# Performance work log

Measured on AMD Instinct MI355X. Metric: run time of the kernel, lower is better.

Reference implementation:

```python
import jax, jax.numpy as jnp
import numpy as np
from jax import lax

VOCAB, EMB, HID = 50257, 256, 256
B, T = 64, 2048

def setup_inputs() -> dict:
    key = jax.random.key(0)
    ks = jax.random.split(key, 6)
    s = 1.0 / np.sqrt(HID)
    return {
        "sequence": jax.random.randint(ks[0], (B, T), 0, VOCAB),
        "embedding": jax.random.normal(ks[1], (VOCAB, EMB), jnp.float32),
        "w_ih": jax.random.uniform(ks[2], (3 * HID, EMB), jnp.float32, -s, s),
        "w_hh": jax.random.uniform(ks[3], (3 * HID, HID), jnp.float32, -s, s),
        "b_ih": jax.random.uniform(ks[4], (3 * HID,), jnp.float32, -s, s),
        "b_hh": jax.random.uniform(ks[5], (3 * HID,), jnp.float32, -s, s),
    }

def reference(sequence, embedding, w_ih, w_hh, b_ih, b_hh):
    # sequence: [B,T] int tokens. Original loops per-timestep; math == one GRU pass.
    H = w_hh.shape[1]
    x = embedding[sequence]                       # [B,T,E]
    x = jnp.transpose(x, (1, 0, 2))               # [T,B,E] (time-major)
    # input-side gate pre-activations for all steps at once: [T,B,3H]
    gi = jnp.einsum('tbe,ge->tbg', x, w_ih) + b_ih

    def step(h, gi_t):
        gh = h @ w_hh.T + b_hh                    # [B,3H]
        i_r, i_z, i_n = jnp.split(gi_t, 3, axis=-1)
        h_r, h_z, h_n = jnp.split(gh, 3, axis=-1)
        r = jax.nn.sigmoid(i_r + h_r)
        z = jax.nn.sigmoid(i_z + h_z)
        n = jnp.tanh(i_n + r * h_n)
        h_new = (1.0 - z) * n + z * h
        return h_new, None

    h0 = jnp.zeros((sequence.shape[0], H), dtype=embedding.dtype)
    hT, _ = lax.scan(step, h0, gi)
    return hT[None]                                # [1,B,H] like torch GRU hidden
```

## Files before the change

### kernel.cpp

```cpp
#include <hip/hip_runtime.h>
#include <hip/hip_fp16.h>

#define TSEQ   2048
#define NB     64
#define NE     256
#define NH     256
#define NG     768
#define TCH    64
#define NCHUNK (TSEQ / TCH)
#define POOL_BYTES 87552

__global__ void prep_whh(const float* __restrict__ whh, unsigned int* __restrict__ w16) {
  int idx = blockIdx.x * 256 + threadIdx.x;
  if (idx >= 98304) return;
  int c  = idx & 3;
  int i  = (idx >> 2) & 15;
  int g  = (idx >> 6) % 3;
  int js = idx / 192;
  int s  = js & 1;
  int j  = js >> 1;
  int k  = s * 128 + i * 8 + 2 * c;
  const float* src = whh + (size_t)(g * 256 + j) * 256 + k;
  union { struct { _Float16 a, b; } h; unsigned int u; } cvt;
  cvt.h.a = (_Float16)src[0];
  cvt.h.b = (_Float16)src[1];
  w16[idx] = cvt.u;
}

#define DOT12(H0,H1,H2,H3,R0,R1,R2,R3,Z0,Z1,Z2,Z3,N0,N1,N2,N3) \
  "v_dot2_f32_f16 v16, v" H0 ", v" R0 ", v16\n\t" \
  "v_dot2_f32_f16 v17, v" H0 ", v" Z0 ", v17\n\t" \
  "v_dot2_f32_f16 v18, v" H0 ", v" N0 ", v18\n\t" \
  "v_dot2_f32_f16 v16, v" H1 ", v" R1 ", v16\n\t" \
  "v_dot2_f32_f16 v17, v" H1 ", v" Z1 ", v17\n\t" \
  "v_dot2_f32_f16 v18, v" H1 ", v" N1 ", v18\n\t" \
  "v_dot2_f32_f16 v16, v" H2 ", v" R2 ", v16\n\t" \
  "v_dot2_f32_f16 v17, v" H2 ", v" Z2 ", v17\n\t" \
  "v_dot2_f32_f16 v18, v" H2 ", v" N2 ", v18\n\t" \
  "v_dot2_f32_f16 v16, v" H3 ", v" R3 ", v16\n\t" \
  "v_dot2_f32_f16 v17, v" H3 ", v" Z3 ", v17\n\t" \
  "v_dot2_f32_f16 v18, v" H3 ", v" N3 ", v18\n\t"

#define TAIL(CA0,CA1,CA2,WOF) \
  "ds_bpermute_b32 v20, v19, v16\n\t" \
  "ds_bpermute_b32 v21, v19, v17\n\t" \
  "ds_bpermute_b32 v22, v19, v18\n\t" \
  "s_waitcnt lgkmcnt(0)\n\t" \
  "v_add_f32 v16, v16, v20\n\t" \
  "v_add_f32 v17, v17, v21\n\t" \
  "v_add_f32 v18, v18, v22\n\t" \
  "s_waitcnt vmcnt(3)\n\t" \
  "v_add_f32 v20, v" CA0 ", v16\n\t" \
  "v_mul_f32 v20, 0xbfb8aa3b, v20\n\t" \
  "v_exp_f32 v20, v20\n\t" \
  "s_nop 0\n\t" \
  "v_add_f32 v20, 1.0, v20\n\t" \
  "v_rcp_f32 v20, v20\n\t" \
  "s_nop 0\n\t" \
  "v_add_f32 v21, v" CA1 ", v17\n\t" \
  "v_mul_f32 v21, 0xbfb8aa3b, v21\n\t" \
  "v_exp_f32 v21, v21\n\t" \
  "s_nop 0\n\t" \
  "v_add_f32 v21, 1.0, v21\n\t" \
  "v_rcp_f32 v21, v21\n\t" \
  "s_nop 0\n\t" \
  "v_add_f32 v22, v18, v28\n\t" \
  "v_fma_f32 v22, v20, v22, v" CA2 "\n\t" \
  "v_min_f32 v22, 0x41700000, v22\n\t" \
  "v_mul_f32 v22, 0x4038aa3b, v22\n\t" \
  "v_exp_f32 v22, v22\n\t" \
  "s_nop 0\n\t" \
  "v_add_f32 v23, -1.0, v22\n\t" \
  "v_add_f32 v22, 1.0, v22\n\t" \
  "v_rcp_f32 v22, v22\n\t" \
  "s_nop 0\n\t" \
  "v_mul_f32 v22, v23, v22\n\t" \
  "v_sub_f32 v23, v24, v22\n\t" \
  "v_fma_f32 v24, v21, v23, v22\n\t" \
  "v_cvt_f16_f32 v25, v24\n\t" \
  "ds_write_b16 v29, v25 offset:" WOF "\n\t" \
  "s_waitcnt lgkmcnt(0)\n\t" \
  "s_barrier\n\t"

#define STEP(O0,O1,O2,O3,O4,O5,O6,O7,O8,O9,O10,O11,O12,O13,O14,O15,CA0,CA1,CA2,PB0,PB1,PB2,WOF) \
  "ds_read_b128 v[32:35], v2 offset:" O0 "\n\t" \
  "ds_read_b128 v[36:39], v2 offset:" O1 "\n\t" \
  "ds_read_b128 v[40:43], v2 offset:" O2 "\n\t" \
  "ds_read_b128 v[44:47], v2 offset:" O3 "\n\t" \
  "ds_read_b128 v[48:51], v2 offset:" O4 "\n\t" \
  "ds_read_b128 v[52:55], v2 offset:" O5 "\n\t" \
  "ds_read_b128 v[56:59], v2 offset:" O6 "\n\t" \
  "ds_read_b128 v[60:63], v2 offset:" O7 "\n\t" \
  "global_load_dword v" PB0 ", v3, %[gip]\n\t" \
  "global_load_dword v" PB1 ", v3, %[gip] offset:1024\n\t" \
  "global_load_dword v" PB2 ", v3, %[gip] offset:2048\n\t" \
  "v_add_u32 v3, 0x30000, v3\n\t" \
  "v_mov_b32 v16, 0\n\t" \
  "v_mov_b32 v17, 0\n\t" \
  "v_mov_b32 v18, 0\n\t" \
  "s_waitcnt lgkmcnt(7)\n\t" \
  DOT12("32","33","34","35","64","65","66","67","128","129","130","131","192","193","194","195") \
  "ds_read_b128 v[32:35], v2 offset:" O8 "\n\t" \
  "s_waitcnt lgkmcnt(7)\n\t" \
  DOT12("36","37","38","39","68","69","70","71","132","133","134","135","196","197","198","199") \
  "ds_read_b128 v[36:39], v2 offset:" O9 "\n\t" \
  "s_waitcnt lgkmcnt(7)\n\t" \
  DOT12("40","41","42","43","72","73","74","75","136","137","138","139","200","201","202","203") \
  "ds_read_b128 v[40:43], v2 offset:" O10 "\n\t" \
  "s_waitcnt lgkmcnt(7)\n\t" \
  DOT12("44","45","46","47","76","77","78","79","140","141","142","143","204","205","206","207") \
  "ds_read_b128 v[44:47], v2 offset:" O11 "\n\t" \
  "s_waitcnt lgkmcnt(7)\n\t" \
  DOT12("48","49","50","51","80","81","82","83","144","145","146","147","208","209","210","211") \
  "ds_read_b128 v[48:51], v2 offset:" O12 "\n\t" \
  "s_waitcnt lgkmcnt(7)\n\t" \
  DOT12("52","53","54","55","84","85","86","87","148","149","150","151","212","213","214","215") \
  "ds_read_b128 v[52:55], v2 offset:" O13 "\n\t" \
  "s_waitcnt lgkmcnt(7)\n\t" \
  DOT12("56","57","58","59","88","89","90","91","152","153","154","155","216","217","218","219") \
  "ds_read_b128 v[56:59], v2 offset:" O14 "\n\t" \
  "s_waitcnt lgkmcnt(7)\n\t" \
  DOT12("60","61","62","63","92","93","94","95","156","157","158","159","220","221","222","223") \
  "ds_read_b128 v[60:63], v2 offset:" O15 "\n\t" \
  "s_waitcnt lgkmcnt(7)\n\t" \
  DOT12("32","33","34","35","96","97","98","99","160","161","162","163","224","225","226","227") \
  "s_waitcnt lgkmcnt(6)\n\t" \
  DOT12("36","37","38","39","100","101","102","103","164","165","166","167","228","229","230","231") \
  "s_waitcnt lgkmcnt(5)\n\t" \
  DOT12("40","41","42","43","104","105","106","107","168","169","170","171","232","233","234","235") \
  "s_waitcnt lgkmcnt(4)\n\t" \
  DOT12("44","45","46","47","108","109","110","111","172","173","174","175","236","237","238","239") \
  "s_waitcnt lgkmcnt(3)\n\t" \
  DOT12("48","49","50","51","112","113","114","115","176","177","178","179","240","241","242","243") \
  "s_waitcnt lgkmcnt(2)\n\t" \
  DOT12("52","53","54","55","116","117","118","119","180","181","182","183","244","245","246","247") \
  "s_waitcnt lgkmcnt(1)\n\t" \
  DOT12("56","57","58","59","120","121","122","123","184","185","186","187","248","249","250","251") \
  "s_waitcnt lgkmcnt(0)\n\t" \
  DOT12("60","61","62","63","124","125","126","127","188","189","190","191","252","253","254","255") \
  TAIL(CA0,CA1,CA2,WOF)

#define WLD(D0,D1,OFF) \
  "global_load_dwordx4 v[" D0 ":" D1 "], %[wof], %[wptr] offset:" OFF "\n\t"

__global__ __launch_bounds__(512)
void fused_kernel(const int* __restrict__ seq, const float* __restrict__ emb,
                  const float* __restrict__ wih, const float* __restrict__ bih,
                  const float* __restrict__ bhh, const unsigned int* __restrict__ w16,
                  const float* __restrict__ rec_gi, float* __restrict__ gi_dst,
                  int gi_t0, float* __restrict__ h_state, float* __restrict__ out,
                  int rec_count, int chunk)
{
  __shared__ __align__(16) char smem[POOL_BYTES];
  const int tid = threadIdx.x;

  if ((int)blockIdx.x < rec_count) {
    const int b = blockIdx.x;
    const unsigned lane = tid & 63;
    const unsigned jj   = (unsigned)(tid >> 6) * 32 + (lane & 31);
    const unsigned sh   = lane >> 5;

    float h0 = 0.f;
    if (chunk != 0) h0 = h_state[b * NH + jj];
    const float bnv = bhh[2 * NH + jj];
    ((_Float16*)smem)[jj] = (_Float16)h0;
    __syncthreads();

    const unsigned pool0 = (unsigned)(uintptr_t)(smem);
    const unsigned hrd = pool0 + sh * 256;
    const unsigned hwa = pool0 + jj * 2;
    const unsigned gio = jj * 4;
    const unsigned bpa = (lane ^ 32u) << 2;
    const unsigned wof = (jj * 2 + sh) * 768;
    const float* gib = rec_gi + (size_t)b * NG;

    float hout;
    asm volatile(
      "v_mov_b32 v2, %[hrd]\n\t"
      "v_mov_b32 v3, %[gio]\n\t"
      "v_mov_b32 v19, %[bpa]\n\t"
      "v_mov_b32 v24, %[h0]\n\t"
      "v_mov_b32 v28, %[bn]\n\t"
      "v_mov_b32 v29, %[hwa]\n\t"
      WLD("64","67","0")    WLD("68","71","16")   WLD("72","75","32")   WLD("76","79","48")
      WLD("80","83","64")   WLD("84","87","80")   WLD("88","91","96")   WLD("92","95","112")
      WLD("96","99","128")  WLD("100","103","144")WLD("104","107","160")WLD("108","111","176")
      WLD("112","115","192")WLD("116","119","208")WLD("120","123","224")WLD("124","127","240")
      WLD("128","131","256")WLD("132","135","272")WLD("136","139","288")WLD("140","143","304")
      WLD("144","147","320")WLD("148","151","336")WLD("152","155","352")WLD("156","159","368")
      WLD("160","163","384")WLD("164","167","400")WLD("168","171","416")WLD("172","175","432")
      WLD("176","179","448")WLD("180","183","464")WLD("184","187","480")WLD("188","191","496")
      WLD("192","195","512")WLD("196","199","528")WLD("200","203","544")WLD("204","207","560")
      WLD("208","211","576")WLD("212","215","592")WLD("216","219","608")WLD("220","223","624")
      WLD("224","227","640")WLD("228","231","656")WLD("232","235","672")WLD("236","239","688")
      WLD("240","243","704")WLD("244","247","720")WLD("248","251","736")WLD("252","255","752")
      "s_waitcnt vmcnt(0)\n\t"
      "global_load_dword v12, v3, %[gip]\n\t"
      "global_load_dword v13, v3, %[gip] offset:1024\n\t"
      "global_load_dword v14, v3, %[gip] offset:2048\n\t"
      "v_add_u32 v3, 0x30000, v3\n\t"
      "s_mov_b32 s20, 32\n\t"
      "1:\n\t"
      STEP("0","16","32","48","64","80","96","112",
           "128","144","160","176","192","208","224","240",
           "12","13","14","26","27","30","512")
      STEP("512","528","544","560","576","592","608","624",
           "640","656","672","688","704","720","736","752",
           "26","27","30","12","13","14","0")
      "s_sub_u32 s20, s20, 1\n\t"
      "s_cmp_lg_u32 s20, 0\n\t"
      "s_cbranch_scc1 1b\n\t"
      "v_mov_b32 %[hout], v24\n\t"
      : [hout] "=v"(hout)
      : [hrd] "v"(hrd), [gio] "v"(gio), [bpa] "v"(bpa), [h0] "v"(h0),
        [bn] "v"(bnv), [hwa] "v"(hwa), [wof] "v"(wof),
        [wptr] "s"(w16), [gip] "s"(gib)
      : "memory","scc","s20",
        "v2","v3","v12","v13","v14","v16","v17","v18","v19","v20","v21","v22",
        "v23","v24","v25","v26","v27","v28","v29","v30",
        "v32","v33","v34","v35","v36","v37","v38","v39","v40","v41","v42","v43",
        "v44","v45","v46","v47","v48","v49","v50","v51","v52","v53","v54","v55",
        "v56","v57","v58","v59","v60","v61","v62","v63",
        "v64","v65","v66","v67","v68","v69","v70","v71","v72","v73","v74","v75",
        "v76","v77","v78","v79","v80","v81","v82","v83","v84","v85","v86","v87",
        "v88","v89","v90","v91","v92","v93","v94","v95","v96","v97","v98","v99",
        "v100","v101","v102","v103","v104","v105","v106","v107","v108","v109",
        "v110","v111","v112","v113","v114","v115","v116","v117","v118","v119",
        "v120","v121","v122","v123","v124","v125","v126","v127","v128","v129",
        "v130","v131","v132","v133","v134","v135","v136","v137","v138","v139",
        "v140","v141","v142","v143","v144","v145","v146","v147","v148","v149",
        "v150","v151","v152","v153","v154","v155","v156","v157","v158","v159",
        "v160","v161","v162","v163","v164","v165","v166","v167","v168","v169",
        "v170","v171","v172","v173","v174","v175","v176","v177","v178","v179",
        "v180","v181","v182","v183","v184","v185","v186","v187","v188","v189",
        "v190","v191","v192","v193","v194","v195","v196","v197","v198","v199",
        "v200","v201","v202","v203","v204","v205","v206","v207","v208","v209",
        "v210","v211","v212","v213","v214","v215","v216","v217","v218","v219",
        "v220","v221","v222","v223","v224","v225","v226","v227","v228","v229",
        "v230","v231","v232","v233","v234","v235","v236","v237","v238","v239",
        "v240","v241","v242","v243","v244","v245","v246","v247","v248","v249",
        "v250","v251","v252","v253","v254","v255");

    h_state[b * NH + jj] = hout;
    if (out) out[b * NH + jj] = hout;
  } else {
    if (gi_dst == nullptr) return;
    float (*xs)[68]  = (float(*)[68])smem;
    float (*wsh)[68] = (float(*)[68])(smem + 17408);
    int*  tok        = (int*)(smem + 17408 + 69632);
    const int gb = blockIdx.x - rec_count;
    const int tl = gb & 63;
    const int g0 = (gb >> 6) * 256;
    const int t  = gi_t0 + tl;
    if (tid < 64) tok[tid] = seq[tid * TSEQ + t];
    const int tx = tid & 31;
    const int ty = tid >> 5;
    float acc[4][8];
#pragma unroll
    for (int i = 0; i < 4; ++i)
#pragma unroll
      for (int c8 = 0; c8 < 8; ++c8) acc[i][c8] = 0.f;

    for (int kb = 0; kb < 4; ++kb) {
      __syncthreads();
#pragma unroll
      for (int it = 0; it < 2; ++it) {
        int i = it * 512 + tid;
        int r = i >> 4, c = i & 15;
        *(float4*)(&xs[r][c * 4]) =
            *(const float4*)(emb + (size_t)tok[r] * NE + kb * 64 + c * 4);
      }
#pragma unroll
      for (int it = 0; it < 8; ++it) {
        int i = it * 512 + tid;
        int r = i >> 4, c = i & 15;
        *(float4*)(&wsh[r][c * 4]) =
            *(const float4*)(wih + (size_t)(g0 + r) * NE + kb * 64 + c * 4);
      }
      __syncthreads();
#pragma unroll 4
      for (int k4 = 0; k4 < 16; ++k4) {
        float4 xf[4], wf[8];
#pragma unroll
        for (int i = 0; i < 4; ++i) xf[i] = *(const float4*)(&xs[ty * 4 + i][k4 * 4]);
#pragma unroll
        for (int c8 = 0; c8 < 8; ++c8) wf[c8] = *(const float4*)(&wsh[tx + 32 * c8][k4 * 4]);
#pragma unroll
        for (int i = 0; i < 4; ++i)
#pragma unroll
          for (int c8 = 0; c8 < 8; ++c8)
            acc[i][c8] += xf[i].x * wf[c8].x + xf[i].y * wf[c8].y +
                          xf[i].z * wf[c8].z + xf[i].w * wf[c8].w;
      }
    }
#pragma unroll
    for (int i = 0; i < 4; ++i) {
      const int brow = ty * 4 + i;
      float* dst = gi_dst + ((size_t)(tl * NB + brow)) * NG + g0;
#pragma unroll
      for (int c8 = 0; c8 < 8; ++c8) {
        const int col = tx + 32 * c8;
        const int g = g0 + col;
        float bias = bih[g] + (g < 2 * NH ? bhh[g] : 0.f);
        dst[col] = acc[i][c8] + bias;
      }
    }
  }
}

extern "C" void kernel_launch(void* const* d_in, const int* in_sizes, int n_in,
                              void* d_out, int out_size, void* d_ws, size_t ws_size,
                              hipStream_t stream) {
  (void)in_sizes; (void)n_in; (void)out_size; (void)ws_size;
  const int*   seq = (const int*)d_in[0];
  const float* emb = (const float*)d_in[1];
  const float* wih = (const float*)d_in[2];
  const float* whh = (const float*)d_in[3];
  const float* bih = (const float*)d_in[4];
  const float* bhh = (const float*)d_in[5];
  float* out = (float*)d_out;
  char*  ws  = (char*)d_ws;

  unsigned int* w16     = (unsigned int*)(ws);
  float*        h_state = (float*)(ws + 393216);
  float*        gi0     = (float*)(ws + 458752);
  float*        gi1     = (float*)(ws + 458752 + 12582912);

  prep_whh<<<dim3(384), dim3(256), 0, stream>>>(whh, w16);

  fused_kernel<<<dim3(192), dim3(512), 0, stream>>>(
      seq, emb, wih, bih, bhh, w16,
      nullptr, gi0, 0, h_state, nullptr, 0, 0);

  for (int c = 0; c < NCHUNK; ++c) {
    float* rd  = (c & 1) ? gi1 : gi0;
    float* wr_ = (c & 1) ? gi0 : gi1;
    const bool last = (c == NCHUNK - 1);
    const int grid  = last ? NB : NB + 192;
    fused_kernel<<<dim3(grid), dim3(512), 0, stream>>>(
        seq, emb, wih, bih, bhh, w16,
        rd, last ? nullptr : wr_, (c + 1) * TCH, h_state,
        last ? out : nullptr, NB, c);
  }
}
```

Baseline: 2.631 ms.

## Split fused recurrence/projection kernel into separate rec and gi kernels

Replaces the single fused kernel, which ran recurrence blocks and next-chunk input-projection blocks in one grid, with two kernels launched back to back per chunk. The recurrence kernel now needs only 2 KB of shared memory instead of the large shared pool. The aim is to stop the projection blocks from contending with the latency-bound recurrence blocks. The cost is that the projection work is no longer overlapped with the recurrence, and the launch count per chunk doubles.

```diff
diff --git a/kernel.cpp b/kernel.cpp
--- a/kernel.cpp
+++ b/kernel.cpp
@@ -8,7 +8,6 @@
 #define NG     768
 #define TCH    64
 #define NCHUNK (TSEQ / TCH)
-#define POOL_BYTES 87552
 
 __global__ void prep_whh(const float* __restrict__ whh, unsigned int* __restrict__ w16) {
   int idx = blockIdx.x * 256 + threadIdx.x;
@@ -144,166 +143,169 @@
   "global_load_dwordx4 v[" D0 ":" D1 "], %[wof], %[wptr] offset:" OFF "\n\t"
 
 __global__ __launch_bounds__(512)
-void fused_kernel(const int* __restrict__ seq, const float* __restrict__ emb,
-                  const float* __restrict__ wih, const float* __restrict__ bih,
-                  const float* __restrict__ bhh, const unsigned int* __restrict__ w16,
-                  const float* __restrict__ rec_gi, float* __restrict__ gi_dst,
-                  int gi_t0, float* __restrict__ h_state, float* __restrict__ out,
-                  int rec_count, int chunk)
+void rec_kernel(const unsigned int* __restrict__ w16,
+                const float* __restrict__ rec_gi,
+                const float* __restrict__ bhh,
+                float* __restrict__ h_state, float* __restrict__ out,
+                int chunk)
 {
-  __shared__ __align__(16) char smem[POOL_BYTES];
+  __shared__ __align__(16) char smem[2048];
   const int tid = threadIdx.x;
-
-  if ((int)blockIdx.x < rec_count) {
-    const int b = blockIdx.x;
-    const unsigned lane = tid & 63;
-    const unsigned jj   = (unsigned)(tid >> 6) * 32 + (lane & 31);
-    const unsigned sh   = lane >> 5;
-
-    float h0 = 0.f;
-    if (chunk != 0) h0 = h_state[b * NH + jj];
-    const float bnv = bhh[2 * NH + jj];
-    ((_Float16*)smem)[jj] = (_Float16)h0;
+  const int b = blockIdx.x;
+  const unsigned lane = tid & 63;
+  const unsigned jj   = (unsigned)(tid >> 6) * 32 + (lane & 31);
+  const unsigned sh   = lane >> 5;
+
+  float h0 = 0.f;
+  if (chunk != 0) h0 = h_state[b * NH + jj];
+  const float bnv = bhh[2 * NH + jj];
+  ((_Float16*)smem)[jj] = (_Float16)h0;
+  __syncthreads();
+
+  const unsigned pool0 = (unsigned)(uintptr_t)(smem);
+  const unsigned hrd = pool0 + sh * 256;
+  const unsigned hwa = pool0 + jj * 2;
+  const unsigned gio = jj * 4;
+  const unsigned bpa = (lane ^ 32u) << 2;
+  const unsigned wof = (jj * 2 + sh) * 768;
+  const float* gib = rec_gi + (size_t)b * NG;
+
+  float hout;
+  asm volatile(
+    "v_mov_b32 v2, %[hrd]\n\t"
+    "v_mov_b32 v3, %[gio]\n\t"
+    "v_mov_b32 v19, %[bpa]\n\t"
+    "v_mov_b32 v24, %[h0]\n\t"
+    "v_mov_b32 v28, %[bn]\n\t"
+    "v_mov_b32 v29, %[hwa]\n\t"
+    WLD("64","67","0")    WLD("68","71","16")   WLD("72","75","32")   WLD("76","79","48")
+    WLD("80","83","64")   WLD("84","87","80")   WLD("88","91","96")   WLD("92","95","112")
+    WLD("96","99","128")  WLD("100","103","144")WLD("104","107","160")WLD("108","111","176")
+    WLD("112","115","192")WLD("116","119","208")WLD("120","123","224")WLD("124","127","240")
+    WLD("128","131","256")WLD("132","135","272")WLD("136","139","288")WLD("140","143","304")
+    WLD("144","147","320")WLD("148","151","336")WLD("152","155","352")WLD("156","159","368")
+    WLD("160","163","384")WLD("164","167","400")WLD("168","171","416")WLD("172","175","432")
+    WLD("176","179","448")WLD("180","183","464")WLD("184","187","480")WLD("188","191","496")
+    WLD("192","195","512")WLD("196","199","528")WLD("200","203","544")WLD("204","207","560")
+    WLD("208","211","576")WLD("212","215","592")WLD("216","219","608")WLD("220","223","624")
+    WLD("224","227","640")WLD("228","231","656")WLD("232","235","672")WLD("236","239","688")
+    WLD("240","243","704")WLD("244","247","720")WLD("248","251","736")WLD("252","255","752")
+    "s_waitcnt vmcnt(0)\n\t"
+    "global_load_dword v12, v3, %[gip]\n\t"
+    "global_load_dword v13, v3, %[gip] offset:1024\n\t"
+    "global_load_dword v14, v3, %[gip] offset:2048\n\t"
+    "v_add_u32 v3, 0x30000, v3\n\t"
+    "s_mov_b32 s20, 32\n\t"
+    "1:\n\t"
+    STEP("0","16","32","48","64","80","96","112",
+         "128","144","160","176","192","208","224","240",
+         "12","13","14","26","27","30","512")
+    STEP("512","528","544","560","576","592","608","624",
+         "640","656","672","688","704","720","736","752",
+         "26","27","30","12","13","14","0")
+    "s_sub_u32 s20, s20, 1\n\t"
+    "s_cmp_lg_u32 s20, 0\n\t"
+    "s_cbranch_scc1 1b\n\t"
+    "v_mov_b32 %[hout], v24\n\t"
+    : [hout] "=v"(hout)
+    : [hrd] "v"(hrd), [gio] "v"(gio), [bpa] "v"(bpa), [h0] "v"(h0),
+      [bn] "v"(bnv), [hwa] "v"(hwa), [wof] "v"(wof),
+      [wptr] "s"(w16), [gip] "s"(gib)
+    : "memory","scc","s20",
+      "v2","v3","v12","v13","v14","v16","v17","v18","v19","v20","v21","v22",
+      "v23","v24","v25","v26","v27","v28","v29","v30",
+      "v32","v33","v34","v35","v36","v37","v38","v39","v40","v41","v42","v43",
+      "v44","v45","v46","v47","v48","v49","v50","v51","v52","v53","v54","v55",
+      "v56","v57","v58","v59","v60","v61","v62","v63",
+      "v64","v65","v66","v67","v68","v69","v70","v71","v72","v73","v74","v75",
+      "v76","v77","v78","v79","v80","v81","v82","v83","v84","v85","v86","v87",
+      "v88","v89","v90","v91","v92","v93","v94","v95","v96","v97","v98","v99",
+      "v100","v101","v102","v103","v104","v105","v106","v107","v108","v109",
+      "v110","v111","v112","v113","v114","v115","v116","v117","v118","v119",
+      "v120","v121","v122","v123","v124","v125","v126","v127","v128","v129",
+      "v130","v131","v132","v133","v134","v135","v136","v137","v138","v139",
+      "v140","v141","v142","v143","v144","v145","v146","v147","v148","v149",
+      "v150","v151","v152","v153","v154","v155","v156","v157","v158","v159",
+      "v160","v161","v162","v163","v164","v165","v166","v167","v168","v169",
+      "v170","v171","v172","v173","v174","v175","v176","v177","v178","v179",
+      "v180","v181","v182","v183","v184","v185","v186","v187","v188","v189",
+      "v190","v191","v192","v193","v194","v195","v196","v197","v198","v199",
+      "v200","v201","v202","v203","v204","v205","v206","v207","v208","v209",
+      "v210","v211","v212","v213","v214","v215","v216","v217","v218","v219",
+      "v220","v221","v222","v223","v224","v225","v226","v227","v228","v229",
+      "v230","v231","v232","v233","v234","v235","v236","v237","v238","v239",
+      "v240","v241","v242","v243","v244","v245","v246","v247","v248","v249",
+      "v250","v251","v252","v253","v254","v255");
+
+  h_state[b * NH + jj] = hout;
+  if (out) out[b * NH + jj] = hout;
+}
+
+__global__ __launch_bounds__(512)
+void gi_kernel(const int* __restrict__ seq, const float* __restrict__ emb,
+               const float* __restrict__ wih, const float* __restrict__ bih,
+               const float* __restrict__ bhh, float* __restrict__ gi_dst,
+               int gi_t0)
+{
+  __shared__ __align__(16) float xs[64][68];
+  __shared__ __align__(16) float wsh[256][68];
+  __shared__ int tok[64];
+  const int tid = threadIdx.x;
+  const int gb = blockIdx.x;
+  const int tl = gb & 63;
+  const int g0 = (gb >> 6) * 256;
+  const int t  = gi_t0 + tl;
+  if (tid < 64) tok[tid] = seq[tid * TSEQ + t];
+  const int tx = tid & 31;
+  const int ty = tid >> 5;
+  float acc[4][8];
+#pragma unroll
+  for (int i = 0; i < 4; ++i)
+#pragma unroll
+    for (int c8 = 0; c8 < 8; ++c8) acc[i][c8] = 0.f;
+
+  for (int kb = 0; kb < 4; ++kb) {
     __syncthreads();
-
-    const unsigned pool0 = (unsigned)(uintptr_t)(smem);
-    const unsigned hrd = pool0 + sh * 256;
-    const unsigned hwa = pool0 + jj * 2;
-    const unsigned gio = jj * 4;
-    const unsigned bpa = (lane ^ 32u) << 2;
-    const unsigned wof = (jj * 2 + sh) * 768;
-    const float* gib = rec_gi + (size_t)b * NG;
-
-    float hout;
-    asm volatile(
-      "v_mov_b32 v2, %[hrd]\n\t"
-      "v_mov_b32 v3, %[gio]\n\t"
-      "v_mov_b32 v19, %[bpa]\n\t"
-      "v_mov_b32 v24, %[h0]\n\t"
-      "v_mov_b32 v28, %[bn]\n\t"
-      "v_mov_b32 v29, %[hwa]\n\t"
-      WLD("64","67","0")    WLD("68","71","16")   WLD("72","75","32")   WLD("76","79","48")
-      WLD("80","83","64")   WLD("84","87","80")   WLD("88","91","96")   WLD("92","95","112")
-      WLD("96","99","128")  WLD("100","103","144")WLD("104","107","160")WLD("108","111","176")
-      WLD("112","115","192")WLD("116","119","208")WLD("120","123","224")WLD("124","127","240")
-      WLD("128","131","256")WLD("132","135","272")WLD("136","139","288")WLD("140","143","304")
-      WLD("144","147","320")WLD("148","151","336")WLD("152","155","352")WLD("156","159","368")
-      WLD("160","163","384")WLD("164","167","400")WLD("168","171","416")WLD("172","175","432")
-      WLD("176","179","448")WLD("180","183","464")WLD("184","187","480")WLD("188","191","496")
-      WLD("192","195","512")WLD("196","199","528")WLD("200","203","544")WLD("204","207","560")
-      WLD("208","211","576")WLD("212","215","592")WLD("216","219","608")WLD("220","223","624")
-      WLD("224","227","640")WLD("228","231","656")WLD("232","235","672")WLD("236","239","688")
-      WLD("240","243","704")WLD("244","247","720")WLD("248","251","736")WLD("252","255","752")
-      "s_waitcnt vmcnt(0)\n\t"
-      "global_load_dword v12, v3, %[gip]\n\t"
-      "global_load_dword v13, v3, %[gip] offset:1024\n\t"
-      "global_load_dword v14, v3, %[gip] offset:2048\n\t"
-      "v_add_u32 v3, 0x30000, v3\n\t"
-      "s_mov_b32 s20, 32\n\t"
-      "1:\n\t"
-      STEP("0","16","32","48","64","80","96","112",
-           "128","144","160","176","192","208","224","240",
-           "12","13","14","26","27","30","512")
-      STEP("512","528","544","560","576","592","608","624",
-           "640","656","672","688","704","720","736","752",
-           "26","27","30","12","13","14","0")
-      "s_sub_u32 s20, s20, 1\n\t"
-      "s_cmp_lg_u32 s20, 0\n\t"
-      "s_cbranch_scc1 1b\n\t"
-      "v_mov_b32 %[hout], v24\n\t"
-      : [hout] "=v"(hout)
-      : [hrd] "v"(hrd), [gio] "v"(gio), [bpa] "v"(bpa), [h0] "v"(h0),
-        [bn] "v"(bnv), [hwa] "v"(hwa), [wof] "v"(wof),
-        [wptr] "s"(w16), [gip] "s"(gib)
-      : "memory","scc","s20",
-        "v2","v3","v12","v13","v14","v16","v17","v18","v19","v20","v21","v22",
-        "v23","v24","v25","v26","v27","v28","v29","v30",
-        "v32","v33","v34","v35","v36","v37","v38","v39","v40","v41","v42","v43",
-        "v44","v45","v46","v47","v48","v49","v50","v51","v52","v53","v54","v55",
-        "v56","v57","v58","v59","v60","v61","v62","v63",
-        "v64","v65","v66","v67","v68","v69","v70","v71","v72","v73","v74","v75",
-        "v76","v77","v78","v79","v80","v81","v82","v83","v84","v85","v86","v87",
-        "v88","v89","v90","v91","v92","v93","v94","v95","v96","v97","v98","v99",
-        "v100","v101","v102","v103","v104","v105","v106","v107","v108","v109",
-        "v110","v111","v112","v113","v114","v115","v116","v117","v118","v119",
-        "v120","v121","v122","v123","v124","v125","v126","v127","v128","v129",
-        "v130","v131","v132","v133","v134","v135","v136","v137","v138","v139",
-        "v140","v141","v142","v143","v144","v145","v146","v147","v148","v149",
-        "v150","v151","v152","v153","v154","v155","v156","v157","v158","v159",
-        "v160","v161","v162","v163","v164","v165","v166","v167","v168","v169",
-        "v170","v171","v172","v173","v174","v175","v176","v177","v178","v179",
-        "v180","v181","v182","v183","v184","v185","v186","v187","v188","v189",
-        "v190","v191","v192","v193","v194","v195","v196","v197","v198","v199",
-        "v200","v201","v202","v203","v204","v205","v206","v207","v208","v209",
-        "v210","v211","v212","v213","v214","v215","v216","v217","v218","v219",
-        "v220","v221","v222","v223","v224","v225","v226","v227","v228","v229",
-        "v230","v231","v232","v233","v234","v235","v236","v237","v238","v239",
-        "v240","v241","v242","v243","v244","v245","v246","v247","v248","v249",
-        "v250","v251","v252","v253","v254","v255");
-
-    h_state[b * NH + jj] = hout;
-    if (out) out[b * NH + jj] = hout;
-  } else {
-    if (gi_dst == nullptr) return;
-    float (*xs)[68]  = (float(*)[68])smem;
-    float (*wsh)[68] = (float(*)[68])(smem + 17408);
-    int*  tok        = (int*)(smem + 17408 + 69632);
-    const int gb = blockIdx.x - rec_count;
-    const int tl = gb & 63;
-    const int g0 = (gb >> 6) * 256;
-    const int t  = gi_t0 + tl;
-    if (tid < 64) tok[tid] = seq[tid * TSEQ + t];
-    const int tx = tid & 31;
-    const int ty = tid >> 5;
-    float acc[4][8];
-#pragma unroll
-    for (int i = 0; i < 4; ++i)
-#pragma unroll
-      for (int c8 = 0; c8 < 8; ++c8) acc[i][c8] = 0.f;
-
-    for (int kb = 0; kb < 4; ++kb) {
-      __syncthreads();
-#pragma unroll
-      for (int it = 0; it < 2; ++it) {
-        int i = it * 512 + tid;
-        int r = i >> 4, c = i & 15;
-        *(float4*)(&xs[r][c * 4]) =
-            *(const float4*)(emb + (size_t)tok[r] * NE + kb * 64 + c * 4);
-      }
-#pragma unroll
-      for (int it = 0; it < 8; ++it) {
-        int i = it * 512 + tid;
-        int r = i >> 4, c = i & 15;
-        *(float4*)(&wsh[r][c * 4]) =
-            *(const float4*)(wih + (size_t)(g0 + r) * NE + kb * 64 + c * 4);
-      }
-      __syncthreads();
+#pragma unroll
+    for (int it = 0; it < 2; ++it) {
+      int i = it * 512 + tid;
+      int r = i >> 4, c = i & 15;
+      *(float4*)(&xs[r][c * 4]) =
+          *(const float4*)(emb + (size_t)tok[r] * NE + kb * 64 + c * 4);
+    }
+#pragma unroll
+    for (int it = 0; it < 8; ++it) {
+      int i = it * 512 + tid;
+      int r = i >> 4, c = i & 15;
+      *(float4*)(&wsh[r][c * 4]) =
+          *(const float4*)(wih + (size_t)(g0 + r) * NE + kb * 64 + c * 4);
+    }
+    __syncthreads();
 #pragma unroll 4
-      for (int k4 = 0; k4 < 16; ++k4) {
-        float4 xf[4], wf[8];
-#pragma unroll
-        for (int i = 0; i < 4; ++i) xf[i] = *(const float4*)(&xs[ty * 4 + i][k4 * 4]);
-#pragma unroll
-        for (int c8 = 0; c8 < 8; ++c8) wf[c8] = *(const float4*)(&wsh[tx + 32 * c8][k4 * 4]);
-#pragma unroll
-        for (int i = 0; i < 4; ++i)
-#pragma unroll
-          for (int c8 = 0; c8 < 8; ++c8)
-            acc[i][c8] += xf[i].x * wf[c8].x + xf[i].y * wf[c8].y +
-                          xf[i].z * wf[c8].z + xf[i].w * wf[c8].w;
-      }
+    for (int k4 = 0; k4 < 16; ++k4) {
+      float4 xf[4], wf[8];
+#pragma unroll
+      for (int i = 0; i < 4; ++i) xf[i] = *(const float4*)(&xs[ty * 4 + i][k4 * 4]);
+#pragma unroll
+      for (int c8 = 0; c8 < 8; ++c8) wf[c8] = *(const float4*)(&wsh[tx + 32 * c8][k4 * 4]);
+#pragma unroll
+      for (int i = 0; i < 4; ++i)
+#pragma unroll
+        for (int c8 = 0; c8 < 8; ++c8)
+          acc[i][c8] += xf[i].x * wf[c8].x + xf[i].y * wf[c8].y +
+                        xf[i].z * wf[c8].z + xf[i].w * wf[c8].w;
     }
-#pragma unroll
-    for (int i = 0; i < 4; ++i) {
-      const int brow = ty * 4 + i;
-      float* dst = gi_dst + ((size_t)(tl * NB + brow)) * NG + g0;
-#pragma unroll
-      for (int c8 = 0; c8 < 8; ++c8) {
-        const int col = tx + 32 * c8;
-        const int g = g0 + col;
-        float bias = bih[g] + (g < 2 * NH ? bhh[g] : 0.f);
-        dst[col] = acc[i][c8] + bias;
-      }
+  }
+#pragma unroll
+  for (int i = 0; i < 4; ++i) {
+    const int brow = ty * 4 + i;
+    float* dst = gi_dst + ((size_t)(tl * NB + brow)) * NG + g0;
+#pragma unroll
+    for (int c8 = 0; c8 < 8; ++c8) {
+      const int col = tx + 32 * c8;
+      const int g = g0 + col;
+      float bias = bih[g] + (g < 2 * NH ? bhh[g] : 0.f);
+      dst[col] = acc[i][c8] + bias;
     }
   }
 }
@@ -328,18 +330,16 @@
 
   prep_whh<<<dim3(384), dim3(256), 0, stream>>>(whh, w16);
 
-  fused_kernel<<<dim3(192), dim3(512), 0, stream>>>(
-      seq, emb, wih, bih, bhh, w16,
-      nullptr, gi0, 0, h_state, nullptr, 0, 0);
+  gi_kernel<<<dim3(192), dim3(512), 0, stream>>>(seq, emb, wih, bih, bhh, gi0, 0);
 
   for (int c = 0; c < NCHUNK; ++c) {
     float* rd  = (c & 1) ? gi1 : gi0;
     float* wr_ = (c & 1) ? gi0 : gi1;
     const bool last = (c == NCHUNK - 1);
-    const int grid  = last ? NB : NB + 192;
-    fused_kernel<<<dim3(grid), dim3(512), 0, stream>>>(
-        seq, emb, wih, bih, bhh, w16,
-        rd, last ? nullptr : wr_, (c + 1) * TCH, h_state,
-        last ? out : nullptr, NB, c);
+    rec_kernel<<<dim3(NB), dim3(512), 0, stream>>>(
+        w16, rd, bhh, h_state, last ? out : nullptr, c);
+    if (!last)
+      gi_kernel<<<dim3(192), dim3(512), 0, stream>>>(
+          seq, emb, wih, bih, bhh, wr_, (c + 1) * TCH);
   }
 }
```

After: 3.897 ms. 1.48x slower.
